# Performance work log

Measured on AMD Instinct MI355X. Metric: run time of the kernel, lower is better.

## Reference

```python
import jax, jax.numpy as jnp
import numpy as np

EPS = 1e-6
FRAME_SEQLEN = 1560          # hardcoded in source kv-cache path
LOCAL_ATTN_SIZE = 4
MAX_ATTN = LOCAL_ATTN_SIZE * FRAME_SEQLEN  # 6240
NUM_HEADS = 12


def _ln(x, w=None, b=None):
    mu = jnp.mean(x, axis=-1, keepdims=True)
    var = jnp.mean(jnp.square(x - mu), axis=-1, keepdims=True)
    y = (x - mu) * jax.lax.rsqrt(var + EPS)
    return y * w + b if w is not None else y


def _rms(x, w):
    return x * jax.lax.rsqrt(jnp.mean(jnp.square(x), axis=-1, keepdims=True) + EPS) * w


def _rope_tables(freqs_real, freqs_imag, nf, hh, ww, start_frame, c):
    # split freqs columns into temporal / height / width parts, as in causal_rope_apply
    s0 = c - 2 * (c // 3)
    s1 = c // 3
    def build(tab):
        f0 = tab[start_frame:start_frame + nf, :s0]       # [nf, s0]
        f1 = tab[:hh, s0:s0 + s1]                          # [hh, s1]
        f2 = tab[:ww, s0 + s1:]                            # [ww, s1]
        return jnp.concatenate([
            jnp.broadcast_to(f0[:, None, None, :], (nf, hh, ww, s0)),
            jnp.broadcast_to(f1[None, :, None, :], (nf, hh, ww, s1)),
            jnp.broadcast_to(f2[None, None, :, :], (nf, hh, ww, s1)),
        ], axis=-1).reshape(nf * hh * ww, 1, c)
    return build(freqs_real), build(freqs_imag)


def _causal_rope(x, cos, sin):
    # x: [B, L, n, d] with interleaved (real, imag) pairs; cos/sin: [1, L, 1, c]
    B, L, n, d = x.shape
    c = d // 2
    xr = x.reshape(B, L, n, c, 2)
    a, b = xr[..., 0], xr[..., 1]
    out = jnp.stack([a * cos - b * sin, a * sin + b * cos], axis=-1)
    return out.reshape(B, L, n, d)


def _sdpa(q, k, v):
    scale = q.shape[-1] ** -0.5
    s = jnp.einsum('bqhd,bkhd->bhqk', q, k) * scale
    a = jax.nn.softmax(s, axis=-1)
    return jnp.einsum('bhqk,bkhd->bqhd', a, v)


def _forward(hidden_states, encoder_hidden_states, temb, freqs_real, freqs_imag,
             k_cache, v_cache, scale_shift_table,
             Wq, bq, Wk, bk, Wv, bv, Wo, bo, norm_q_w, norm_k_w,
             saln_w, saln_b,
             cWq, cbq, cWk, cbk, cWv, cbv, cWo, cbo, c_norm_q_w, c_norm_k_w,
             W1, b1, W2, b2,
             current_start, grid_h, grid_w):
    B, L, D = hidden_states.shape
    nf = temb.shape[1]
    fs = L // nf                     # == FRAME_SEQLEN
    H = NUM_HEADS
    hd = D // H
    c = hd // 2
    x = hidden_states.astype(jnp.float32)

    # AdaLN modulation per frame
    e = scale_shift_table + temb                     # [B, nf, 6, D]
    shift, scale, gate = e[:, :, 0:1], e[:, :, 1:2], e[:, :, 2:3]
    c_shift, c_scale, c_gate = e[:, :, 3:4], e[:, :, 4:5], e[:, :, 5:6]

    nh = (_ln(x).reshape(B, nf, fs, D) * (1 + scale) + shift).reshape(B, L, D)

    # self-attn projections + rms_norm_across_heads qk norm
    q = _rms(nh @ Wq.T + bq, norm_q_w).reshape(B, L, H, hd)
    k = _rms(nh @ Wk.T + bk, norm_k_w).reshape(B, L, H, hd)
    v = (nh @ Wv.T + bv).reshape(B, L, H, hd)

    # causal RoPE with temporal offset current_start // 1560
    start_frame = current_start // FRAME_SEQLEN
    cos, sin = _rope_tables(freqs_real, freqs_imag, nf, grid_h, grid_w, start_frame, c)
    cos, sin = cos[None], sin[None]                  # [1, L, 1, c]
    rq = _causal_rope(q, cos, sin)
    rk = _causal_rope(k, cos, sin)

    # kv-cache update (no-eviction branch: num_new + local_end_prev == cache size)
    kc = jax.lax.stop_gradient(k_cache).at[:, current_start:current_start + L].set(rk)
    vc = jax.lax.stop_gradient(v_cache).at[:, current_start:current_start + L].set(v)
    local_end = current_start + L
    win_lo = max(0, local_end - MAX_ATTN)
    attn = _sdpa(rq, kc[:, win_lo:local_end], vc[:, win_lo:local_end]).reshape(B, L, D)
    attn = attn @ Wo.T + bo

    # gated residual + affine LN (self_attn_residual_norm)
    x = x + (attn.reshape(B, nf, fs, D) * gate).reshape(B, L, D)
    n2 = _ln(x, saln_w, saln_b)

    # T2V cross attention
    ctx = encoder_hidden_states.astype(jnp.float32)
    Lc = ctx.shape[1]
    cq = _rms(n2 @ cWq.T + cbq, c_norm_q_w).reshape(B, L, H, hd)
    ck = _rms(ctx @ cWk.T + cbk, c_norm_k_w).reshape(B, Lc, H, hd)
    cv = (ctx @ cWv.T + cbv).reshape(B, Lc, H, hd)
    ca = _sdpa(cq, ck, cv).reshape(B, L, D) @ cWo.T + cbo

    # residual + LN with c_scale/c_shift modulation (cross_attn_residual_norm)
    x = x + ca
    n3 = (_ln(x).reshape(B, nf, fs, D) * (1 + c_scale) + c_shift).reshape(B, L, D)

    # FFN (gelu tanh) + gated residual (MulAdd)
    ff = jax.nn.gelu(n3 @ W1.T + b1, approximate=True) @ W2.T + b2
    x = x + (ff.reshape(B, nf, fs, D) * c_gate).reshape(B, L, D)
    return x


def setup_inputs() -> dict:
    key = jax.random.key(0)
    D, FF, H = 1536, 8960, NUM_HEADS
    NF, FS = 2, FRAME_SEQLEN
    L = NF * FS
    CACHE = MAX_ATTN
    CTX = 512
    hd = D // H
    c = hd // 2
    ks = iter(jax.random.split(key, 40))
    def nrm(shape, s=1.0):
        return jax.random.normal(next(ks), shape, jnp.float32) * s

    def part(dim):
        inv = 1.0 / (10000.0 ** (np.arange(0, dim, 2, dtype=np.float64) / dim))
        f = np.outer(np.arange(1024, dtype=np.float64), inv)
        return np.cos(f), np.sin(f)
    c0, s0 = part(2 * (c - 2 * (c // 3)))
    c1, s1 = part(2 * (c // 3))
    c2, s2 = part(2 * (c // 3))
    freqs_real = jnp.asarray(np.concatenate([c0, c1, c2], axis=1), jnp.float32)  # [1024, 64]
    freqs_imag = jnp.asarray(np.concatenate([s0, s1, s2], axis=1), jnp.float32)

    return dict(
        hidden_states=nrm((1, L, D)),
        encoder_hidden_states=nrm((1, CTX, D)),
        temb=nrm((1, NF, 6, D), 0.5),
        freqs_real=freqs_real, freqs_imag=freqs_imag,
        k_cache=nrm((1, CACHE, H, hd), 0.5),
        v_cache=nrm((1, CACHE, H, hd), 0.5),
        scale_shift_table=nrm((1, 6, D), D ** -0.5),
        Wq=nrm((D, D), 0.02), bq=jnp.zeros((D,), jnp.float32),
        Wk=nrm((D, D), 0.02), bk=jnp.zeros((D,), jnp.float32),
        Wv=nrm((D, D), 0.02), bv=jnp.zeros((D,), jnp.float32),
        Wo=nrm((D, D), 0.02), bo=jnp.zeros((D,), jnp.float32),
        norm_q_w=jnp.ones((D,), jnp.float32), norm_k_w=jnp.ones((D,), jnp.float32),
        saln_w=jnp.ones((D,), jnp.float32), saln_b=jnp.zeros((D,), jnp.float32),
        cWq=nrm((D, D), 0.02), cbq=jnp.zeros((D,), jnp.float32),
        cWk=nrm((D, D), 0.02), cbk=jnp.zeros((D,), jnp.float32),
        cWv=nrm((D, D), 0.02), cbv=jnp.zeros((D,), jnp.float32),
        cWo=nrm((D, D), 0.02), cbo=jnp.zeros((D,), jnp.float32),
        c_norm_q_w=jnp.ones((D,), jnp.float32), c_norm_k_w=jnp.ones((D,), jnp.float32),
        W1=nrm((FF, D), 0.02), b1=jnp.zeros((FF,), jnp.float32),
        W2=nrm((D, FF), 0.02), b2=jnp.zeros((D,), jnp.float32),
        current_start=2 * FS, grid_h=30, grid_w=52,
    )


def reference(hidden_states, encoder_hidden_states, temb, freqs_real, freqs_imag,
              k_cache, v_cache, scale_shift_table,
              Wq, bq, Wk, bk, Wv, bv, Wo, bo, norm_q_w, norm_k_w,
              saln_w, saln_b,
              cWq, cbq, cWk, cbk, cWv, cbv, cWo, cbo, c_norm_q_w, c_norm_k_w,
              W1, b1, W2, b2,
              current_start, grid_h, grid_w):
    return _forward(hidden_states, encoder_hidden_states, temb, freqs_real, freqs_imag,
                    k_cache, v_cache, scale_shift_table,
                    Wq, bq, Wk, bk, Wv, bv, Wo, bo, norm_q_w, norm_k_w,
                    saln_w, saln_b,
                    cWq, cbq, cWk, cbk, cWv, cbv, cWo, cbo, c_norm_q_w, c_norm_k_w,
                    W1, b1, W2, b2,
                    current_start, grid_h, grid_w)
```

## Files before the change

kernel.cpp:

```cpp
#include <hip/hip_runtime.h>
#include <hip/hip_bf16.h>
#include <stdint.h>

typedef uint16_t u16;
typedef uint32_t u32;
typedef float    f32x4  __attribute__((ext_vector_type(4)));
typedef __bf16   bf16x8 __attribute__((ext_vector_type(8)));
typedef u16      u16x8  __attribute__((ext_vector_type(8)));
typedef u16      u16x4  __attribute__((ext_vector_type(4)));
typedef float    f32x4v __attribute__((ext_vector_type(4)));


__device__ __forceinline__ u16 f2bf(float f) {
    u32 u = __builtin_bit_cast(u32, f);
    u32 r = u + 0x7fffu + ((u >> 16) & 1u);
    return (u16)(r >> 16);
}
__device__ __forceinline__ float bfbits2f(u32 ubits) {
    return __builtin_bit_cast(float, ubits << 16);
}
__device__ __forceinline__ u32 cvtpk(float a, float b) {
    u32 r;
    asm("v_cvt_pk_bf16_f32 %0, %1, %2" : "=v"(r) : "v"(a), "v"(b));
    return r;
}
__device__ __forceinline__ bf16x8 loadb8(const u16* p) {
    u16x8 u = *(const u16x8*)p;
    return __builtin_bit_cast(bf16x8, u);
}
__device__ __forceinline__ f32x4 mfma16(bf16x8 a, bf16x8 b, f32x4 c) {
    return __builtin_amdgcn_mfma_f32_16x16x32_bf16(a, b, c, 0, 0, 0);
}
__device__ __forceinline__ void gload16(const u16* gp, u16* lp) {
    __builtin_amdgcn_global_load_lds((const __attribute__((address_space(1))) void*)gp,
                                     (__attribute__((address_space(3))) void*)lp, 16, 0, 0);
}
__device__ __forceinline__ float blockSum(float v, volatile float* buf, int t) {
#pragma unroll
    for (int o = 1; o < 64; o <<= 1) v += __shfl_xor(v, o);
    if ((t & 63) == 0) buf[t >> 6] = v;
    __syncthreads();
    float r = buf[0] + buf[1] + buf[2] + buf[3];
    __syncthreads();
    return r;
}

struct ConvJob { const float* s; u16* d; int n4; };
struct ConvJobs { ConvJob j[12]; int cnt; };

__global__ void k_conv(ConvJobs js) {
    int tid = blockIdx.x * blockDim.x + threadIdx.x;
    int stride = gridDim.x * blockDim.x;
    for (int q = 0; q < js.cnt; q++) {
        const f32x4v* s = (const f32x4v*)js.j[q].s;
        u16x4* d = (u16x4*)js.j[q].d;
        int n4 = js.j[q].n4;
        for (int i = tid; i < n4; i += stride) {
            f32x4v v = s[i];
            u16x4 o;
            o[0] = f2bf(v[0]); o[1] = f2bf(v[1]); o[2] = f2bf(v[2]); o[3] = f2bf(v[3]);
            d[i] = o;
        }
    }
}

__global__ void k_mod(const float* __restrict__ sst, const float* __restrict__ temb, float* __restrict__ e) {
    int i = blockIdx.x * 256 + threadIdx.x;
    if (i < 18432) e[i] = sst[i % 9216] + temb[i];
}

__global__ void k_cachecvt(const float* __restrict__ kc, const float* __restrict__ vc,
                           u16* __restrict__ Ka, u16* __restrict__ Va) {
    int b = blockIdx.x;
    int hd = (b % 6) * 256 + threadIdx.x;
    int p0 = (b / 6) * 16;
    int h = hd >> 7, d = hd & 127;
    u16x8 lo, hi;
#pragma unroll
    for (int j = 0; j < 16; j++) {
        long src = (long)(p0 + j) * 1536 + hd;
        Ka[(long)h * 798720 + (long)(p0 + j) * 128 + d] = f2bf(kc[src]);
        u16 v = f2bf(vc[src]);
        if (j < 8) lo[j] = v; else hi[j - 8] = v;
    }
    u16* dst = &Va[(long)h * 798720 + (long)d * 6240 + p0];
    *(u16x8*)dst = lo;
    *(u16x8*)(dst + 8) = hi;
}

__global__ __launch_bounds__(256) void k_ln(const float* __restrict__ x, u16* __restrict__ out,
                                            const float* __restrict__ mulp, const float* __restrict__ addp,
                                            int perFrame, int plusOne) {
    __shared__ float buf[4];
    const int row = blockIdx.x, t = threadIdx.x;
    const float* xr = x + (long)row * 1536;
    float v[6];
    float s = 0.f;
#pragma unroll
    for (int k = 0; k < 6; k++) { v[k] = xr[t + k * 256]; s += v[k]; }
    s = blockSum(s, buf, t);
    float mu = s * (1.f / 1536.f);
    float q = 0.f;
#pragma unroll
    for (int k = 0; k < 6; k++) { float d = v[k] - mu; q += d * d; }
    q = blockSum(q, buf, t);
    float inv = rsqrtf(q * (1.f / 1536.f) + 1e-6f);
    const int fo = perFrame ? (row / 1560) * 9216 : 0;
    u16* orow = out + (long)row * 1536;
    float add1 = plusOne ? 1.f : 0.f;
#pragma unroll
    for (int k = 0; k < 6; k++) {
        int c = t + k * 256;
        float m = mulp[fo + c] + add1;
        float y = (v[k] - mu) * inv * m + addp[fo + c];
        orow[c] = f2bf(y);
    }
}

__global__ __launch_bounds__(256) void k_rmsrope(const u16* __restrict__ in, int ld, int colOff,
                                                 const float* __restrict__ bias,
                                                 const float* __restrict__ w,
                                                 u16* __restrict__ out, long headStride,
                                                 const float* __restrict__ fr, const float* __restrict__ fi,
                                                 int doRope) {
    __shared__ float buf[4];
    const int row = blockIdx.x, t = threadIdx.x;
    const u32* xr = (const u32*)(in + (long)row * ld + colOff);
    const float2* b2 = (const float2*)bias;
    float px[3], py[3];
    float ss = 0.f;
#pragma unroll
    for (int i = 0; i < 3; i++) {
        u32 u = xr[t * 3 + i];
        float2 bb = b2[t * 3 + i];
        px[i] = bfbits2f(u & 0xffffu) + bb.x;
        py[i] = bfbits2f(u >> 16) + bb.y;
        ss += px[i] * px[i] + py[i] * py[i];
    }
    ss = blockSum(ss, buf, t);
    float inv = rsqrtf(ss * (1.f / 1536.f) + 1e-6f);
    int frame = 0, gh = 0, gw = 0;
    if (doRope) { frame = row / 1560; int rem = row - frame * 1560; gh = rem / 52; gw = rem - gh * 52; }
    const float2* w2 = (const float2*)w;
#pragma unroll
    for (int i = 0; i < 3; i++) {
        int jg = t * 3 + i;
        int hh = jg >> 6, j = jg & 63;
        float2 ww = w2[jg];
        float a = px[i] * inv * ww.x, b = py[i] * inv * ww.y;
        float oa = a, ob = b;
        if (doRope) {
            int fidx = (j < 22) ? (2 + frame) : ((j < 43) ? gh : gw);
            float cs = fr[fidx * 64 + j], sn = fi[fidx * 64 + j];
            oa = a * cs - b * sn;
            ob = a * sn + b * cs;
        }
        u16* dst = out + (long)hh * headStride + (long)row * 128 + j * 2;
        dst[0] = f2bf(oa);
        dst[1] = f2bf(ob);
    }
}

__global__ void k_scatterT(const u16* __restrict__ in, int ld, int colOff,
                           const float* __restrict__ bias, u16* __restrict__ outT,
                           int vstride, int posOff) {
    int hd = blockIdx.x * 256 + threadIdx.x;
    int r0 = blockIdx.y * 16;
    int h = hd >> 7, d = hd & 127;
    float bi = bias[hd];
    u16x8 lo, hi;
#pragma unroll
    for (int j = 0; j < 16; j++) {
        u16 v = f2bf(bfbits2f(in[(long)(r0 + j) * ld + colOff + hd]) + bi);
        if (j < 8) lo[j] = v; else hi[j - 8] = v;
    }
    u16* dst = &outT[(long)h * 128 * vstride + (long)d * vstride + posOff + r0];
    *(u16x8*)dst = lo;
    *(u16x8*)(dst + 8) = hi;
}

struct GemmP {
    const u16* A; const u16* B; void* C;
    const float* bias; const float* gate; const float* resid;
    int M, N, K, ldA, ldB, ldC, kChunk;
};

template <int EPI, int BM>
__global__ __launch_bounds__(256) void k_gemm(GemmP g) {
    constexpr int WM = BM / 2;
    constexpr int TM = BM / 32;
    __shared__ alignas(16) u16 As[BM * 32];
    __shared__ alignas(16) u16 Bs[128 * 32];
    const int t = threadIdx.x;
    const int w = t >> 6, l = t & 63, lr = l & 15, lg = l >> 4;
    const int wm = w >> 1, wn = w & 1;
    const long m0 = (long)blockIdx.y * BM, n0 = (long)blockIdx.x * 128;
    f32x4 acc[TM][4];
#pragma unroll
    for (int a = 0; a < TM; a++)
#pragma unroll
        for (int b = 0; b < 4; b++) acc[a][b] = f32x4{0.f, 0.f, 0.f, 0.f};

    const int rowU = t >> 2, c8 = t & 3;
    long arow[2], brow[2];
#pragma unroll
    for (int i = 0; i < 2; i++) {
        long r = m0 + rowU + i * 64;
        if (r > (long)g.M - 1) r = g.M - 1;
        arow[i] = r;
        brow[i] = n0 + rowU + i * 64;
    }

    const int kBeg = blockIdx.z * g.kChunk;
    const int kEnd = min(g.K, kBeg + g.kChunk);
    for (int k0 = kBeg; k0 < kEnd; k0 += 32) {
        __syncthreads();
#pragma unroll
        for (int i = 0; i < BM / 64; i++)
            gload16(g.A + arow[i] * (long)g.ldA + k0 + c8 * 8, &As[(i * 256 + w * 64) * 8]);
#pragma unroll
        for (int i = 0; i < 2; i++)
            gload16(g.B + brow[i] * (long)g.ldB + k0 + c8 * 8, &Bs[(i * 256 + w * 64) * 8]);
        __syncthreads();
        bf16x8 am[TM], bn[4];
#pragma unroll
        for (int mi = 0; mi < TM; mi++) am[mi] = loadb8(&As[(wm * WM + mi * 16 + lr) * 32 + lg * 8]);
#pragma unroll
        for (int ni = 0; ni < 4; ni++) bn[ni] = loadb8(&Bs[(wn * 64 + ni * 16 + lr) * 32 + lg * 8]);
#pragma unroll
        for (int mi = 0; mi < TM; mi++)
#pragma unroll
            for (int ni = 0; ni < 4; ni++)
                acc[mi][ni] = mfma16(am[mi], bn[ni], acc[mi][ni]);
    }

#pragma unroll
    for (int mi = 0; mi < TM; mi++) {
#pragma unroll
        for (int ni = 0; ni < 4; ni++) {
            long col = n0 + wn * 64 + ni * 16 + lr;
            float bi = g.bias ? g.bias[col] : 0.f;
#pragma unroll
            for (int r = 0; r < 4; r++) {
                long row = m0 + wm * WM + mi * 16 + lg * 4 + r;
                if (row >= g.M) continue;
                float v = acc[mi][ni][r] + bi;
                if constexpr (EPI == 0) {
                    ((float*)g.C)[row * g.ldC + col] = v;
                } else if constexpr (EPI == 1) {
                    ((u16*)g.C)[row * g.ldC + col] = f2bf(v);
                } else if constexpr (EPI == 2) {
                    float x3 = v * v * v;
                    float gl = 0.5f * v * (1.f + tanhf(0.79788456080286536f * (v + 0.044715f * x3)));
                    ((u16*)g.C)[row * g.ldC + col] = f2bf(gl);
                } else if constexpr (EPI == 3) {
                    float gt = g.gate ? g.gate[(row / 1560) * 9216 + col] : 1.f;
                    ((float*)g.C)[row * g.ldC + col] = g.resid[row * g.ldC + col] + v * gt;
                } else {
                    ((float*)g.C)[(long)blockIdx.z * ((long)g.M * g.ldC) + row * g.ldC + col] = v;
                }
            }
        }
    }
}

__global__ void k_gcomb(const float* __restrict__ P, int S, long MN4,
                        const float* __restrict__ bias, const float* __restrict__ gate,
                        const float* __restrict__ resid, float* __restrict__ out) {
    long i = (long)blockIdx.x * 256 + threadIdx.x;
    if (i >= MN4) return;
    f32x4v a = ((const f32x4v*)P)[i];
#pragma unroll 3
    for (int s = 1; s < S; s++) {
        f32x4v b = ((const f32x4v*)P)[(long)s * MN4 + i];
        a[0] += b[0]; a[1] += b[1]; a[2] += b[2]; a[3] += b[3];
    }
    long e0 = i * 4;
    int col = (int)(e0 % 1536);
    int fo = (int)((e0 / 1536) / 1560) * 9216;
    f32x4v r = ((const f32x4v*)resid)[i];
#pragma unroll
    for (int j = 0; j < 4; j++)
        r[j] += (a[j] + bias[col + j]) * gate[fo + col + j];
    ((f32x4v*)out)[i] = r;
}

__global__ void k_sumbf(const float* __restrict__ P, int S, long N4, u16* __restrict__ out) {
    long i = (long)blockIdx.x * 256 + threadIdx.x;
    if (i >= N4) return;
    f32x4v a = ((const f32x4v*)P)[i];
#pragma unroll 3
    for (int s = 1; s < S; s++) {
        f32x4v b = ((const f32x4v*)P)[(long)s * N4 + i];
        a[0] += b[0]; a[1] += b[1]; a[2] += b[2]; a[3] += b[3];
    }
    u16x4 o;
    o[0] = f2bf(a[0]); o[1] = f2bf(a[1]); o[2] = f2bf(a[2]); o[3] = f2bf(a[3]);
    ((u16x4*)out)[i] = o;
}

__global__ __launch_bounds__(256) void k_flash(const u16* __restrict__ Qb, const u16* __restrict__ Kb,
                                               const u16* __restrict__ Vtg,
                                               u16* __restrict__ Opart, float2* __restrict__ ms,
                                               int kvLen, int qlen, int splitIters, int totIters) {
    __shared__ alignas(16) u16 Kt[32 * 136];
    __shared__ alignas(16) u16 Vt[128 * 40];
    __shared__ alignas(16) u16 Pt[4][32 * 40];
    const int t = threadIdx.x;
    const int w = t >> 6, l = t & 63, lr = l & 15, lg = l >> 4;
    const int head = blockIdx.y, z = blockIdx.z;
    const long q0 = (long)blockIdx.x * 128;
    const u16* Qh = Qb + (long)head * qlen * 128;
    const u16* Kh = Kb + (long)head * kvLen * 128;
    const u16* Vh = Vtg + (long)head * kvLen * 128;
    constexpr float SCL2 = 0.08838834764831845f * 1.44269504088896f;

    bf16x8 aq[2][4];
#pragma unroll
    for (int wq = 0; wq < 2; wq++)
#pragma unroll
        for (int c = 0; c < 4; c++) {
            long row = q0 + w * 32 + wq * 16 + lr;
            if (row > (long)qlen - 1) row = qlen - 1;
            aq[wq][c] = loadb8(Qh + row * 128 + c * 32 + lg * 8);
        }

    f32x4 o[2][8];
    float mrow[2] = {-1e30f, -1e30f}, srow[2] = {0.f, 0.f};
#pragma unroll
    for (int wq = 0; wq < 2; wq++)
#pragma unroll
        for (int db = 0; db < 8; db++) o[wq][db] = f32x4{0.f, 0.f, 0.f, 0.f};

    const int kr = t >> 4, c16 = (t & 15) * 8;
    const int vr = t >> 1, vh = (t & 1) * 16;

    const int it0 = z * splitIters;
    const int itN = min(totIters, it0 + splitIters);
    for (int kt = it0; kt < itN; kt++) {
        const long k0 = (long)kt * 32;
        __syncthreads();
        {
            u16x8 a0 = *(const u16x8*)(Kh + (k0 + kr) * 128 + c16);
            u16x8 a1 = *(const u16x8*)(Kh + (k0 + kr + 16) * 128 + c16);
            *(u16x8*)&Kt[kr * 136 + c16] = a0;
            *(u16x8*)&Kt[(kr + 16) * 136 + c16] = a1;
            u16x8 b0 = *(const u16x8*)(Vh + (long)vr * kvLen + k0 + vh);
            u16x8 b1 = *(const u16x8*)(Vh + (long)vr * kvLen + k0 + vh + 8);
            *(u16x8*)&Vt[vr * 40 + vh] = b0;
            *(u16x8*)&Vt[vr * 40 + vh + 8] = b1;
        }
        __syncthreads();

        f32x4 s[2][2];
#pragma unroll
        for (int kh = 0; kh < 2; kh++) {
            bf16x8 kf[4];
#pragma unroll
            for (int cb = 0; cb < 4; cb++)
                kf[cb] = loadb8(&Kt[(kh * 16 + lr) * 136 + cb * 32 + lg * 8]);
#pragma unroll
            for (int wq = 0; wq < 2; wq++) {
                f32x4 acc = f32x4{0.f, 0.f, 0.f, 0.f};
#pragma unroll
                for (int cb = 0; cb < 4; cb++) acc = mfma16(kf[cb], aq[wq][cb], acc);
                s[wq][kh] = acc;
            }
        }

#pragma unroll
        for (int wq = 0; wq < 2; wq++) {
            float pm = fmaxf(fmaxf(fmaxf(s[wq][0][0], s[wq][0][1]), fmaxf(s[wq][0][2], s[wq][0][3])),
                             fmaxf(fmaxf(s[wq][1][0], s[wq][1][1]), fmaxf(s[wq][1][2], s[wq][1][3])));
            pm = fmaxf(pm, __shfl_xor(pm, 16));
            pm = fmaxf(pm, __shfl_xor(pm, 32));
            float pm2 = pm * SCL2;
            if (__any(pm2 > mrow[wq] + 8.f)) {
                float nm = fmaxf(mrow[wq], pm2);
                float fsc = exp2f(mrow[wq] - nm);
                mrow[wq] = nm;
                srow[wq] *= fsc;
#pragma unroll
                for (int db = 0; db < 8; db++) {
                    f32x4 t4 = o[wq][db];
                    t4[0] *= fsc; t4[1] *= fsc; t4[2] *= fsc; t4[3] *= fsc;
                    o[wq][db] = t4;
                }
            }
            float p[8];
#pragma unroll
            for (int kh = 0; kh < 2; kh++)
#pragma unroll
                for (int r = 0; r < 4; r++)
                    p[kh * 4 + r] = exp2f(fmaf(s[wq][kh][r], SCL2, -mrow[wq]));
            float ts = ((p[0] + p[1]) + (p[2] + p[3])) + ((p[4] + p[5]) + (p[6] + p[7]));
            ts += __shfl_xor(ts, 16);
            ts += __shfl_xor(ts, 32);
            srow[wq] += ts;
            u32 w0 = cvtpk(p[0], p[1]), w1 = cvtpk(p[2], p[3]);
            u32 w2 = cvtpk(p[4], p[5]), w3 = cvtpk(p[6], p[7]);
            u16* pp = &Pt[w][(wq * 16 + lr) * 40 + lg * 4];
            *(u32*)pp = w0;
            *(u32*)(pp + 2) = w1;
            *(u32*)(pp + 16) = w2;
            *(u32*)(pp + 18) = w3;
        }

        bf16x8 pb0 = loadb8(&Pt[w][lr * 40 + lg * 8]);
        bf16x8 pb1 = loadb8(&Pt[w][(16 + lr) * 40 + lg * 8]);
#pragma unroll
        for (int db = 0; db < 8; db++) {
            bf16x8 vf = loadb8(&Vt[(db * 16 + lr) * 40 + lg * 8]);
            o[0][db] = mfma16(vf, pb0, o[0][db]);
            o[1][db] = mfma16(vf, pb1, o[1][db]);
        }
    }

    const long part = ((long)z * 12 + head) * qlen;
#pragma unroll
    for (int wq = 0; wq < 2; wq++) {
        long row = q0 + w * 32 + wq * 16 + lr;
        if (row < qlen) {
            if (lg == 0) {
                float2 v; v.x = mrow[wq]; v.y = srow[wq];
                ms[part + row] = v;
            }
#pragma unroll
            for (int db = 0; db < 8; db++) {
                u16x4 pk;
#pragma unroll
                for (int r = 0; r < 4; r++) pk[r] = f2bf(o[wq][db][r]);
                *(u16x4*)&Opart[(part + row) * 128 + db * 16 + lg * 4] = pk;
            }
        }
    }
}

__global__ __launch_bounds__(256) void k_combine(const u16* __restrict__ Opart, const float2* __restrict__ ms,
                                                 u16* __restrict__ Ob, int qlen, int S) {
    int idx = blockIdx.x * 4 + (threadIdx.x >> 6);
    int l = threadIdx.x & 63;
    int h = idx / qlen, q = idx - h * qlen;
    float2 mm[6];
    float M = -1e30f;
    for (int s = 0; s < S; s++) {
        mm[s] = ms[((long)s * 12 + h) * qlen + q];
        M = fmaxf(M, mm[s].x);
    }
    float den = 0.f, a0 = 0.f, a1 = 0.f;
    for (int s = 0; s < S; s++) {
        float wgt = exp2f(mm[s].x - M);
        den += wgt * mm[s].y;
        u32 two = *(const u32*)&Opart[(((long)s * 12 + h) * qlen + q) * 128 + l * 2];
        a0 += wgt * bfbits2f(two & 0xffffu);
        a1 += wgt * bfbits2f(two >> 16);
    }
    float inv = 1.f / den;
    u32 o = ((u32)f2bf(a1 * inv) << 16) | (u32)f2bf(a0 * inv);
    *(u32*)&Ob[(long)q * 1536 + h * 128 + l * 2] = o;
}

extern "C" void kernel_launch(void* const* d_in, const int* in_sizes, int n_in,
                              void* d_out, int out_size, void* d_ws, size_t ws_size,
                              hipStream_t stream) {
    const float* hs    = (const float*)d_in[0];
    const float* ctx   = (const float*)d_in[1];
    const float* temb  = (const float*)d_in[2];
    const float* fr    = (const float*)d_in[3];
    const float* fi    = (const float*)d_in[4];
    const float* kcache= (const float*)d_in[5];
    const float* vcache= (const float*)d_in[6];
    const float* sst   = (const float*)d_in[7];
    const float* Wq = (const float*)d_in[8],  *bq = (const float*)d_in[9];
    const float* Wk = (const float*)d_in[10], *bk = (const float*)d_in[11];
    const float* Wv = (const float*)d_in[12], *bv = (const float*)d_in[13];
    const float* Wo = (const float*)d_in[14], *bo = (const float*)d_in[15];
    const float* nqw = (const float*)d_in[16], *nkw = (const float*)d_in[17];
    const float* salnw = (const float*)d_in[18], *salnb = (const float*)d_in[19];
    const float* cWq = (const float*)d_in[20], *cbq = (const float*)d_in[21];
    const float* cWk = (const float*)d_in[22], *cbk = (const float*)d_in[23];
    const float* cWv = (const float*)d_in[24], *cbv = (const float*)d_in[25];
    const float* cWo = (const float*)d_in[26], *cbo = (const float*)d_in[27];
    const float* cnqw = (const float*)d_in[28], *cnkw = (const float*)d_in[29];
    const float* W1 = (const float*)d_in[30], *b1 = (const float*)d_in[31];
    const float* W2 = (const float*)d_in[32], *b2 = (const float*)d_in[33];
    float* out = (float*)d_out;

    char* base = (char*)d_ws;
    size_t off = 0;
    auto alloc = [&](size_t bytes) -> char* {
        char* p = base + off;
        off = (off + bytes + 255) & ~(size_t)255;
        return p;
    };
    float* e   = (float*)alloc(18432 * 4);
    u16* nbuf  = (u16*)alloc((size_t)3120 * 1536 * 2);
    u16* lin   = (u16*)alloc((size_t)3120 * 4608 * 2);
    u16* Qb    = (u16*)alloc((size_t)12 * 3120 * 128 * 2);
    u16* Ka    = (u16*)alloc((size_t)12 * 6240 * 128 * 2);
    u16* Va    = (u16*)alloc((size_t)12 * 6240 * 128 * 2);
    u16* attnb = (u16*)alloc((size_t)3120 * 1536 * 2);
    float* X1  = (float*)alloc((size_t)3120 * 1536 * 4);
    u16* CKb   = (u16*)alloc((size_t)12 * 512 * 128 * 2);
    u16* CVt   = (u16*)alloc((size_t)12 * 512 * 128 * 2);
    u16* H1    = (u16*)alloc((size_t)3120 * 8960 * 2);
    u16* wqkv_b= (u16*)alloc((size_t)4608 * 1536 * 2);
    u16* wo_b  = (u16*)alloc((size_t)1536 * 1536 * 2);
    u16* cwq_b = (u16*)alloc((size_t)1536 * 1536 * 2);
    u16* cwkv_b= (u16*)alloc((size_t)3072 * 1536 * 2);
    u16* cwo_b = (u16*)alloc((size_t)1536 * 1536 * 2);
    u16* w1_b  = (u16*)alloc((size_t)8960 * 1536 * 2);
    u16* w2_b  = (u16*)alloc((size_t)8960 * 1536 * 2);
    u16* ctxb  = (u16*)alloc((size_t)512 * 1536 * 2);

    u16* Opart = H1;
    float2* msb = (float2*)lin;
    float* pbuf = (float*)lin;
    float* cpart = (float*)H1;

    ConvJobs cj{};
    auto setj = [&](int i, const float* s, u16* d, int n) { cj.j[i].s = s; cj.j[i].d = d; cj.j[i].n4 = n / 4; };
    setj(0, Wq, wqkv_b, 1536 * 1536);
    setj(1, Wk, wqkv_b + (size_t)1536 * 1536, 1536 * 1536);
    setj(2, Wv, wqkv_b + (size_t)2 * 1536 * 1536, 1536 * 1536);
    setj(3, Wo, wo_b, 1536 * 1536);
    setj(4, cWq, cwq_b, 1536 * 1536);
    setj(5, cWk, cwkv_b, 1536 * 1536);
    setj(6, cWv, cwkv_b + (size_t)1536 * 1536, 1536 * 1536);
    setj(7, cWo, cwo_b, 1536 * 1536);
    setj(8, W1, w1_b, 8960 * 1536);
    setj(9, W2, w2_b, 8960 * 1536);
    setj(10, ctx, ctxb, 512 * 1536);
    cj.cnt = 11;
    k_conv<<<2048, 256, 0, stream>>>(cj);

    k_mod<<<72, 256, 0, stream>>>(sst, temb, e);
    k_cachecvt<<<1170, 256, 0, stream>>>(kcache, vcache, Ka, Va);

    k_ln<<<3120, 256, 0, stream>>>(hs, nbuf, e + 1536, e + 0, 1, 1);

    GemmP gqkv{nbuf, wqkv_b, lin, nullptr, nullptr, nullptr, 3120, 4608, 1536, 1536, 1536, 4608, 1536};
    k_gemm<1, 128><<<dim3(36, 25), 256, 0, stream>>>(gqkv);
    k_rmsrope<<<3120, 256, 0, stream>>>(lin, 4608, 0, bq, nqw, Qb, (long)3120 * 128, fr, fi, 1);
    k_rmsrope<<<3120, 256, 0, stream>>>(lin, 4608, 1536, bk, nkw, Ka + (size_t)3120 * 128, (long)6240 * 128, fr, fi, 1);
    k_scatterT<<<dim3(6, 195), 256, 0, stream>>>(lin, 4608, 3072, bv, Va, 6240, 3120);

    k_flash<<<dim3(25, 12, 5), 256, 0, stream>>>(Qb, Ka, Va, Opart, msb, 6240, 3120, 39, 195);
    k_combine<<<9360, 256, 0, stream>>>(Opart, msb, attnb, 3120, 5);

    GemmP gwo{attnb, wo_b, X1, bo, e + 2 * 1536, hs, 3120, 1536, 1536, 1536, 1536, 1536, 1536};
    k_gemm<3, 64><<<dim3(12, 49), 256, 0, stream>>>(gwo);

    k_ln<<<3120, 256, 0, stream>>>(X1, nbuf, salnw, salnb, 0, 0);

    GemmP gcq{nbuf, cwq_b, lin, nullptr, nullptr, nullptr, 3120, 1536, 1536, 1536, 1536, 1536, 1536};
    k_gemm<1, 64><<<dim3(12, 49), 256, 0, stream>>>(gcq);
    k_rmsrope<<<3120, 256, 0, stream>>>(lin, 1536, 0, cbq, cnqw, Qb, (long)3120 * 128, fr, fi, 0);

    GemmP gckv{ctxb, cwkv_b, cpart, nullptr, nullptr, nullptr, 512, 3072, 1536, 1536, 1536, 3072, 384};
    k_gemm<5, 64><<<dim3(24, 8, 4), 256, 0, stream>>>(gckv);
    k_sumbf<<<1536, 256, 0, stream>>>(cpart, 4, 393216, lin);
    k_rmsrope<<<512, 256, 0, stream>>>(lin, 3072, 0, cbk, cnkw, CKb, (long)512 * 128, fr, fi, 0);
    k_scatterT<<<dim3(6, 32), 256, 0, stream>>>(lin, 3072, 1536, cbv, CVt, 512, 0);

    k_flash<<<dim3(25, 12, 4), 256, 0, stream>>>(Qb, CKb, CVt, Opart, msb, 512, 3120, 4, 16);
    k_combine<<<9360, 256, 0, stream>>>(Opart, msb, attnb, 3120, 4);

    GemmP gcwo{attnb, cwo_b, X1, cbo, nullptr, X1, 3120, 1536, 1536, 1536, 1536, 1536, 1536};
    k_gemm<3, 64><<<dim3(12, 49), 256, 0, stream>>>(gcwo);

    k_ln<<<3120, 256, 0, stream>>>(X1, nbuf, e + 4 * 1536, e + 3 * 1536, 1, 1);

    GemmP g1{nbuf, w1_b, H1, b1, nullptr, nullptr, 3120, 8960, 1536, 1536, 1536, 8960, 1536};
    k_gemm<2, 128><<<dim3(70, 25), 256, 0, stream>>>(g1);

    GemmP g2{H1, w2_b, pbuf, nullptr, nullptr, nullptr, 3120, 1536, 8960, 8960, 8960, 1536, 2240};
    k_gemm<5, 128><<<dim3(12, 25, 4), 256, 0, stream>>>(g2);
    k_gcomb<<<4680, 256, 0, stream>>>(pbuf, 4, 1198080, b2, e + 5 * 1536, X1, out);
}
```

Before: 1.086 ms.

## Retile QKV and FFN-down GEMMs, defer flash row-sum reduction, vectorize P stores

The QKV GEMM switches from 128-row to 64-row tiles, giving more blocks. The W2 GEMM also moves to 64-row tiles and halves split-K from 4 to 2, so fewer partials are written and combined. In the flash kernel, the per-tile cross-lane reduction of the softmax sum moves to after the loop, and the row-max shuffle only runs when a rescale is needed; the P tile stores are packed into 64-bit writes. The trade-offs are lower per-block reuse in the retiled GEMMs and longer K loops per block for W2.

```diff
diff --git a/kernel.cpp b/kernel.cpp
--- a/kernel.cpp
+++ b/kernel.cpp
@@ -8,6 +8,7 @@
 typedef __bf16   bf16x8 __attribute__((ext_vector_type(8)));
 typedef u16      u16x8  __attribute__((ext_vector_type(8)));
 typedef u16      u16x4  __attribute__((ext_vector_type(4)));
+typedef u32      u32x2  __attribute__((ext_vector_type(2)));
 typedef float    f32x4v __attribute__((ext_vector_type(4)));
 
 
@@ -270,7 +271,6 @@
     long i = (long)blockIdx.x * 256 + threadIdx.x;
     if (i >= MN4) return;
     f32x4v a = ((const f32x4v*)P)[i];
-#pragma unroll 3
     for (int s = 1; s < S; s++) {
         f32x4v b = ((const f32x4v*)P)[(long)s * MN4 + i];
         a[0] += b[0]; a[1] += b[1]; a[2] += b[2]; a[3] += b[3];
@@ -370,13 +370,12 @@
 
 #pragma unroll
         for (int wq = 0; wq < 2; wq++) {
-            float pm = fmaxf(fmaxf(fmaxf(s[wq][0][0], s[wq][0][1]), fmaxf(s[wq][0][2], s[wq][0][3])),
-                             fmaxf(fmaxf(s[wq][1][0], s[wq][1][1]), fmaxf(s[wq][1][2], s[wq][1][3])));
-            pm = fmaxf(pm, __shfl_xor(pm, 16));
-            pm = fmaxf(pm, __shfl_xor(pm, 32));
-            float pm2 = pm * SCL2;
-            if (__any(pm2 > mrow[wq] + 8.f)) {
-                float nm = fmaxf(mrow[wq], pm2);
+            float pml = fmaxf(fmaxf(fmaxf(s[wq][0][0], s[wq][0][1]), fmaxf(s[wq][0][2], s[wq][0][3])),
+                              fmaxf(fmaxf(s[wq][1][0], s[wq][1][1]), fmaxf(s[wq][1][2], s[wq][1][3])));
+            if (__any(pml * SCL2 > mrow[wq] + 8.f)) {
+                float pm = fmaxf(pml, __shfl_xor(pml, 16));
+                pm = fmaxf(pm, __shfl_xor(pm, 32));
+                float nm = fmaxf(mrow[wq], pm * SCL2);
                 float fsc = exp2f(mrow[wq] - nm);
                 mrow[wq] = nm;
                 srow[wq] *= fsc;
@@ -393,17 +392,13 @@
 #pragma unroll
                 for (int r = 0; r < 4; r++)
                     p[kh * 4 + r] = exp2f(fmaf(s[wq][kh][r], SCL2, -mrow[wq]));
-            float ts = ((p[0] + p[1]) + (p[2] + p[3])) + ((p[4] + p[5]) + (p[6] + p[7]));
-            ts += __shfl_xor(ts, 16);
-            ts += __shfl_xor(ts, 32);
-            srow[wq] += ts;
-            u32 w0 = cvtpk(p[0], p[1]), w1 = cvtpk(p[2], p[3]);
-            u32 w2 = cvtpk(p[4], p[5]), w3 = cvtpk(p[6], p[7]);
+            srow[wq] += ((p[0] + p[1]) + (p[2] + p[3])) + ((p[4] + p[5]) + (p[6] + p[7]));
+            u32x2 wa, wb;
+            wa[0] = cvtpk(p[0], p[1]); wa[1] = cvtpk(p[2], p[3]);
+            wb[0] = cvtpk(p[4], p[5]); wb[1] = cvtpk(p[6], p[7]);
             u16* pp = &Pt[w][(wq * 16 + lr) * 40 + lg * 4];
-            *(u32*)pp = w0;
-            *(u32*)(pp + 2) = w1;
-            *(u32*)(pp + 16) = w2;
-            *(u32*)(pp + 18) = w3;
+            *(u32x2*)pp = wa;
+            *(u32x2*)(pp + 16) = wb;
         }
 
         bf16x8 pb0 = loadb8(&Pt[w][lr * 40 + lg * 8]);
@@ -414,6 +409,12 @@
             o[0][db] = mfma16(vf, pb0, o[0][db]);
             o[1][db] = mfma16(vf, pb1, o[1][db]);
         }
+    }
+
+#pragma unroll
+    for (int wq = 0; wq < 2; wq++) {
+        srow[wq] += __shfl_xor(srow[wq], 16);
+        srow[wq] += __shfl_xor(srow[wq], 32);
     }
 
     const long part = ((long)z * 12 + head) * qlen;
@@ -540,7 +541,7 @@
     k_ln<<<3120, 256, 0, stream>>>(hs, nbuf, e + 1536, e + 0, 1, 1);
 
     GemmP gqkv{nbuf, wqkv_b, lin, nullptr, nullptr, nullptr, 3120, 4608, 1536, 1536, 1536, 4608, 1536};
-    k_gemm<1, 128><<<dim3(36, 25), 256, 0, stream>>>(gqkv);
+    k_gemm<1, 64><<<dim3(36, 49), 256, 0, stream>>>(gqkv);
     k_rmsrope<<<3120, 256, 0, stream>>>(lin, 4608, 0, bq, nqw, Qb, (long)3120 * 128, fr, fi, 1);
     k_rmsrope<<<3120, 256, 0, stream>>>(lin, 4608, 1536, bk, nkw, Ka + (size_t)3120 * 128, (long)6240 * 128, fr, fi, 1);
     k_scatterT<<<dim3(6, 195), 256, 0, stream>>>(lin, 4608, 3072, bv, Va, 6240, 3120);
@@ -574,7 +575,7 @@
     GemmP g1{nbuf, w1_b, H1, b1, nullptr, nullptr, 3120, 8960, 1536, 1536, 1536, 8960, 1536};
     k_gemm<2, 128><<<dim3(70, 25), 256, 0, stream>>>(g1);
 
-    GemmP g2{H1, w2_b, pbuf, nullptr, nullptr, nullptr, 3120, 1536, 8960, 8960, 8960, 1536, 2240};
-    k_gemm<5, 128><<<dim3(12, 25, 4), 256, 0, stream>>>(g2);
-    k_gcomb<<<4680, 256, 0, stream>>>(pbuf, 4, 1198080, b2, e + 5 * 1536, X1, out);
-}
+    GemmP g2{H1, w2_b, pbuf, nullptr, nullptr, nullptr, 3120, 1536, 8960, 8960, 8960, 1536, 4480};
+    k_gemm<5, 64><<<dim3(12, 49, 2), 256, 0, stream>>>(g2);
+    k_gcomb<<<4680, 256, 0, stream>>>(pbuf, 2, 1198080, b2, e + 5 * 1536, X1, out);
+}
```

Result: faster. 1.064 ms (-2.1%).
